# Kernel tuning notes

Measured on AMD Instinct MI355X. Metric: run time of the kernel, lower is better.

The kernel has to match this reference:

```python
import jax, jax.numpy as jnp
import numpy as np

IN_CH = 64
NODE = 48
K_NEIGS = 10
KERNEL = 5
STRIDE = 2
BN_EPS = 1e-5


def _local_kernel(size, k, s):
    idx = np.arange(size * size).reshape(size, size)
    win = np.lib.stride_tricks.sliding_window_view(idx, (k, k))[::s, ::s]
    patches = win.reshape(-1, k * k)  # [n_edges, k*k] pixel indices
    n_edges = patches.shape[0]
    H = np.zeros((size * size, n_edges), dtype=np.float32)
    H[patches.reshape(-1), np.repeat(np.arange(n_edges), k * k)] = 1.0
    return jnp.asarray(H)


def _pairwise_distance(x):
    # (B,N,C) -> (B,N,N) squared euclidean
    xsq = jnp.sum(x * x, axis=-1, keepdims=True)
    return xsq - 2.0 * jnp.einsum('bnc,bmc->bnm', x, x) + jnp.swapaxes(xsq, 1, 2)


def _batched_knn(x, k):
    d = _pairwise_distance(x)
    avg = d.mean(-1, keepdims=True)
    neg_vals, inds = jax.lax.top_k(-d, k + 1)  # smallest k+1, sorted ascending
    return -neg_vals, inds, d, avg


def _incidence(inds, N):
    # weights_function(prob=False) == ones; scatter ones then transpose
    B, _, K = inds.shape
    b = jnp.arange(B)[:, None, None]
    p = jnp.arange(N)[None, :, None]
    M = jnp.zeros((B, N, N), dtype=jnp.float32).at[b, p, inds].set(1.0)
    return jnp.swapaxes(M, 1, 2)


def _generate_G(H):
    # G = diag(DV^-0.5) @ H @ I @ diag(DE^-1) @ H^T @ diag(DV^-0.5)
    DV = H.sum(axis=2)  # (B,N)
    DE = H.sum(axis=1)  # (B,E)
    dv2 = DV ** -0.5
    Hs = H * (1.0 / DE)[:, None, :]
    M = jnp.einsum('bne,bme->bnm', Hs, H)
    return dv2[:, :, None] * M * dv2[:, None, :]


def _build_G(x, local_H):
    B, N, C = x.shape
    _, topk_inds, _, _ = _batched_knn(x, K_NEIGS)
    H1 = _incidence(topk_inds, N)
    Dv = H1.sum(axis=2, keepdims=True)  # alpha = 1.0
    max_k = int(jnp.max(Dv))  # data-dependent width (eager, matches torch)
    _, ti2, _, _ = _batched_knn(x, max_k - 1)  # (B,N,max_k)
    tk = jnp.arange(max_k)[None, None, :]
    rng = jnp.broadcast_to(jnp.arange(N)[None, :, None], (B, N, max_k))
    new_inds = jnp.where(tk >= Dv, rng, ti2)
    new_H = _incidence(new_inds, N)
    loc = jnp.broadcast_to(local_H[None], (B,) + local_H.shape)
    return _generate_G(jnp.concatenate([new_H, loc], axis=2))


def _hgnn(x, G, W, b, gamma, beta):
    h = jnp.einsum('bnc,oc->bno', x, W) + b  # Linear
    h = jnp.einsum('bnm,bmc->bnc', G, h)
    mean = h.mean(axis=(0, 1))  # BatchNorm1d over (B,N) per channel
    var = h.var(axis=(0, 1))
    h = gamma * (h - mean) / jnp.sqrt(var + BN_EPS) + beta
    return jax.nn.relu(h) + x


def setup_inputs() -> dict:
    key = jax.random.key(0)
    k1, k2, k3 = jax.random.split(key, 3)
    B, N, C = 4, NODE * NODE, IN_CH
    x = jax.random.normal(k1, (B, N, C), dtype=jnp.float32)
    W = jax.random.normal(k2, (C, C), dtype=jnp.float32) / np.sqrt(C)
    b = jax.random.normal(k3, (C,), dtype=jnp.float32) * 0.01
    gamma = jnp.ones((C,), dtype=jnp.float32)
    beta = jnp.zeros((C,), dtype=jnp.float32)
    return {"x": x, "W": W, "b": b, "gamma": gamma, "beta": beta}


def reference(x, W, b, gamma, beta):
    local_H = _local_kernel(NODE, KERNEL, STRIDE)
    G = _build_G(x, local_H)  # graph construction is no_grad in torch
    return _hgnn(x, G, W, b, gamma, beta)
```

## Files before the change

### kernel.cpp

```cpp
#include <hip/hip_runtime.h>


#define HB    4
#define HN    2304
#define HC    64
#define HK    11
#define HL    48
#define HW    22
#define HE2   484
#define HE    (HN + HE2)
#define HRPB  4
#define NSLOT 36
#define HCAP4 256
#define NPAIRS (HB * HK * HN)

__global__ void hg17_sentinel(float* out, int n) {
    int i = blockIdx.x * 256 + threadIdx.x;
    if (i < n) out[i] = 12345.0f;
}

__global__ void hg17_init(int* Dv, int* indeg, int* needfb, float* bnsum, float* bnss) {
    int i = blockIdx.x * 256 + threadIdx.x;
    if (i < HB * HN) { Dv[i] = 0; indeg[i] = 0; needfb[i] = 0; }
    if (i < HC) { bnsum[i] = 0.f; bnss[i] = 0.f; }
}

__global__ __launch_bounds__(256) void hg17_linear(const float* x, const float* W,
                                                   const float* bias, float* h1,
                                                   float* xsq, float* xT) {
    int wv = threadIdx.x >> 6, lane = threadIdx.x & 63;
    int row = blockIdx.x * 4 + wv;
    __shared__ float xr[4][HC];
    float v = x[row * HC + lane];
    xr[wv][lane] = v;
    __syncthreads();
    float sq = v * v;
    #pragma unroll
    for (int o = 32; o > 0; o >>= 1) sq += __shfl_xor(sq, o);
    if (lane == 0) xsq[row] = sq;
    int b = row / HN, n = row % HN;
    xT[(b * HC + lane) * HN + n] = v;
    float acc = bias[lane];
    #pragma unroll 8
    for (int c = 0; c < HC; c++) acc += xr[wv][c] * W[lane * HC + c];
    h1[row * HC + lane] = acc;
}

__device__ __forceinline__ unsigned hg17_wave_min_u32(unsigned v) {
    #pragma unroll
    for (int o = 32; o > 0; o >>= 1) {
        unsigned ov = __shfl_xor(v, o);
        v = ov < v ? ov : v;
    }
    return v;
}

#define HG17_INS4(q0, q1, q2, q3, x)                                     \
    {                                                                    \
        unsigned long long x_ = (x), n_;                                 \
        n_ = q0 < x_ ? q0 : x_; x_ = q0 < x_ ? x_ : q0; q0 = n_;         \
        n_ = q1 < x_ ? q1 : x_; x_ = q1 < x_ ? x_ : q1; q1 = n_;         \
        n_ = q2 < x_ ? q2 : x_; x_ = q2 < x_ ? x_ : q2; q2 = n_;         \
        if (x_ < q3) q3 = x_;                                            \
    }

#define HG17_CE(u, v)                                                    \
    { unsigned long long t_ = u < v ? u : v; v = u < v ? v : u; u = t_; }

#define HG17_BUILD()                                                               \
    {                                                                              \
        unsigned long long a0 = CINF, a1 = CINF, a2 = CINF, a3 = CINF;             \
        unsigned long long b0 = CINF, b1 = CINF, b2 = CINF, b3 = CINF;             \
        _Pragma("unroll")                                                          \
        for (int s = 0; s < NSLOT / 2; s++) {                                      \
            unsigned long long pa = ((unsigned long long)key[s] << 12) |           \
                                    (unsigned)((s << 6) | lane);                   \
            unsigned long long pb = ((unsigned long long)key[s + 18] << 12) |      \
                                    (unsigned)(((s + 18) << 6) | lane);            \
            HG17_INS4(a0, a1, a2, a3, pa);                                         \
            HG17_INS4(b0, b1, b2, b3, pb);                                         \
        }                                                                          \
        c0 = a0 < b3 ? a0 : b3; c1 = a1 < b2 ? a1 : b2;                            \
        c2 = a2 < b1 ? a2 : b1; c3 = a3 < b0 ? a3 : b0;                            \
        HG17_CE(c0, c2); HG17_CE(c1, c3); HG17_CE(c0, c1); HG17_CE(c2, c3);        \
    }

#define HG17_EXTRACT(kk, EMIT)                                                     \
    {                                                                              \
        for (int j = 0; j < (kk); j++) {                                           \
            unsigned hk = (unsigned)(c0 >> 12);                                    \
            unsigned mk = hg17_wave_min_u32(hk);                                   \
            unsigned long long bal = __ballot(hk == mk);                           \
            bool iswin;                                                            \
            if (__popcll(bal) == 1) {                                              \
                iswin = (hk == mk);                                                \
            } else {                                                               \
                unsigned mc = (hk == mk) ? (unsigned)(c0 & 0xFFFu) : 0xFFFFFFFFu;  \
                unsigned mm = hg17_wave_min_u32(mc);                               \
                iswin = (mc == mm);                                                \
            }                                                                      \
            if (iswin) {                                                           \
                int bi = (int)(c0 & 0xFFFu);                                       \
                EMIT;                                                              \
                unsigned long long popped = c0;                                    \
                c0 = c1; c1 = c2; c2 = c3; c3 = CINF;                              \
                if (c0 == CINF) {                                                  \
                    _Pragma("unroll")                                              \
                    for (int s = 0; s < NSLOT; s++) {                              \
                        unsigned long long pk =                                    \
                            ((unsigned long long)key[s] << 12) |                   \
                            (unsigned)((s << 6) | lane);                           \
                        if (pk > popped) HG17_INS4(c0, c1, c2, c3, pk);            \
                    }                                                              \
                }                                                                  \
            }                                                                      \
        }                                                                          \
    }

template <int NS>
__device__ __forceinline__ void hg17_kth(const unsigned (&key)[NS], int kk,
                                         unsigned& T, int& cntLess, int& take) {
    unsigned andv = 0xFFFFFFFFu, orv = 0u;
    #pragma unroll
    for (int s = 0; s < NS; s++) { andv &= key[s]; orv |= key[s]; }
    #pragma unroll
    for (int o = 32; o > 0; o >>= 1) {
        andv &= (unsigned)__shfl_xor((int)andv, o);
        orv  |= (unsigned)__shfl_xor((int)orv, o);
    }
    unsigned diff = andv ^ orv;
    if (diff == 0u) { T = andv; cntLess = 0; take = kk; return; }
    int tstart = 31 - __builtin_clz(diff);
    unsigned lowmask = (tstart == 31) ? 0xFFFFFFFFu : ((1u << (tstart + 1)) - 1u);
    unsigned pref = andv & ~lowmask;
    int r = kk;
    for (int t = tstart; t >= 0; t--) {
        unsigned pt = pref >> t;
        int c = 0;
        #pragma unroll
        for (int s = 0; s < NS; s++) c += ((key[s] >> t) == pt) ? 1 : 0;
        #pragma unroll
        for (int o = 32; o > 0; o >>= 1) c += __shfl_xor(c, o);
        if (r > c) { r -= c; pref |= (1u << t); }
    }
    T = pref; cntLess = kk - r; take = r;
}

__device__ __forceinline__ void hg17_scan64(int v, int lane, int& excl, int& total) {
    int inc = v;
    #pragma unroll
    for (int o = 1; o < 64; o <<= 1) {
        int u = __shfl_up(inc, o);
        if (lane >= o) inc += u;
    }
    excl = inc - v;
    total = __shfl(inc, 63);
}

__global__ __launch_bounds__(256) void hg17_knn_count(const float* xT, const float* xsq,
                                                      int* Dv, unsigned long long* topc) {
    __shared__ float d[HRPB][HN];
    __shared__ __align__(16) float xrt[HC][HRPB];
    const int t = threadIdx.x;
    const int b = blockIdx.x / (HN / HRPB);
    const int n0 = (blockIdx.x % (HN / HRPB)) * HRPB;
    const int r = t >> 6;
    const int lane = t & 63;
    xrt[lane][r] = xT[(b * HC + lane) * HN + n0 + r];
    __syncthreads();
    float xs[HRPB];
    #pragma unroll
    for (int q = 0; q < HRPB; q++) xs[q] = xsq[b * HN + n0 + q];

    #pragma unroll
    for (int i = 0; i < 4; i++) {
        const int m = 512 * i + 2 * t;
        float2 d0 = {0.f, 0.f}, d1 = {0.f, 0.f}, d2 = {0.f, 0.f}, d3 = {0.f, 0.f};
        #pragma unroll 8
        for (int c = 0; c < HC; c++) {
            float4 xq = *reinterpret_cast<const float4*>(&xrt[c][0]);
            float2 xv = *reinterpret_cast<const float2*>(&xT[(b * HC + c) * HN + m]);
            d0.x += xq.x * xv.x; d0.y += xq.x * xv.y;
            d1.x += xq.y * xv.x; d1.y += xq.y * xv.y;
            d2.x += xq.z * xv.x; d2.y += xq.z * xv.y;
            d3.x += xq.w * xv.x; d3.y += xq.w * xv.y;
        }
        float s0 = xsq[b * HN + m], s1 = xsq[b * HN + m + 1];
        *reinterpret_cast<float2*>(&d[0][m]) =
            make_float2(xs[0] + s0 - 2.f * d0.x, xs[0] + s1 - 2.f * d0.y);
        *reinterpret_cast<float2*>(&d[1][m]) =
            make_float2(xs[1] + s0 - 2.f * d1.x, xs[1] + s1 - 2.f * d1.y);
        *reinterpret_cast<float2*>(&d[2][m]) =
            make_float2(xs[2] + s0 - 2.f * d2.x, xs[2] + s1 - 2.f * d2.y);
        *reinterpret_cast<float2*>(&d[3][m]) =
            make_float2(xs[3] + s0 - 2.f * d3.x, xs[3] + s1 - 2.f * d3.y);
    }
    {
        const int m = 2048 + t;
        float d0 = 0.f, d1 = 0.f, d2 = 0.f, d3 = 0.f;
        #pragma unroll 8
        for (int c = 0; c < HC; c++) {
            float4 xq = *reinterpret_cast<const float4*>(&xrt[c][0]);
            float xv = xT[(b * HC + c) * HN + m];
            d0 += xq.x * xv; d1 += xq.y * xv; d2 += xq.z * xv; d3 += xq.w * xv;
        }
        float sm = xsq[b * HN + m];
        d[0][m] = xs[0] + sm - 2.f * d0;
        d[1][m] = xs[1] + sm - 2.f * d1;
        d[2][m] = xs[2] + sm - 2.f * d2;
        d[3][m] = xs[3] + sm - 2.f * d3;
    }
    __syncthreads();

    const int p = n0 + r;
    const int gw = b * HN + p;
    const unsigned long long CINF = ~0ull;
    unsigned int key[NSLOT];
    unsigned long long c0, c1, c2, c3;
    #pragma unroll
    for (int s = 0; s < NSLOT; s++) {
        float f = d[r][(s << 6) | lane];
        unsigned int ub = __float_as_uint(f);
        key[s] = ub ^ (((unsigned int)(((int)ub) >> 31)) | 0x80000000u);
    }
    HG17_BUILD();
    {
        unsigned long long* tb = topc + (size_t)gw * HCAP4;
        tb[lane]       = c0;
        tb[64 + lane]  = c1;
        tb[128 + lane] = c2;
        tb[192 + lane] = c3;
    }
    HG17_EXTRACT(HK, atomicAdd(&Dv[b * HN + bi], 1));
}

__global__ __launch_bounds__(256) void hg17_scan(const int* Dv, int* offs) {
    __shared__ int part[256];
    int t = threadIdx.x;
    int base = t * 36;
    int s = 0;
    for (int i = 0; i < 36; i++) s += max(Dv[base + i], 1);
    part[t] = s;
    __syncthreads();
    if (t == 0) { int acc = 0; for (int i = 0; i < 256; i++) { int v = part[i]; part[i] = acc; acc += v; } }
    __syncthreads();
    int acc = part[t];
    for (int i = 0; i < 36; i++) { offs[base + i] = acc; acc += max(Dv[base + i], 1); }
}

__global__ __launch_bounds__(256) void hg17_sel_top(const unsigned long long* topc,
                                                    const int* Dv, const int* offs,
                                                    int* needfb, int* indeg,
                                                    unsigned int* pairs) {
    const int t = threadIdx.x;
    const int lane = t & 63;
    const int gw = blockIdx.x * HRPB + (t >> 6);
    const int b = gw / HN, p = gw % HN;
    const int kk = max(Dv[gw], 1);
    unsigned long long pk[4];
    unsigned key[4];
    #pragma unroll
    for (int s = 0; s < 4; s++) {
        pk[s] = topc[(size_t)gw * HCAP4 + (s << 6) + lane];
        key[s] = (unsigned)(pk[s] >> 12);
    }
    if (kk > HCAP4) {
        if (lane == 0) needfb[gw] = 1;
        return;
    }
    unsigned T; int cntLess, take;
    hg17_kth<4>(key, kk, T, cntLess, take);
    unsigned long long bad = __ballot(key[3] <= T);
    if (bad != 0ull) {
        if (lane == 0) needfb[gw] = 1;
        return;
    }
    const int base = offs[gw];
    int cl = 0;
    #pragma unroll
    for (int s = 0; s < 4; s++) cl += (key[s] < T) ? 1 : 0;
    int off, tot;
    hg17_scan64(cl, lane, off, tot);
    int w = 0;
    #pragma unroll
    for (int s = 0; s < 4; s++) {
        if (key[s] < T) {
            int m = (int)(pk[s] & 0xFFFu);
            atomicAdd(&indeg[b * HN + m], 1);
            pairs[base + off + w] =
                ((unsigned)b << 24) | ((unsigned)p << 12) | (unsigned)m;
            w++;
        }
    }
    int lastm = -1;
    for (int t2 = 0; t2 < take; t2++) {
        int mc = 0x7FFFFFFF;
        #pragma unroll
        for (int s = 0; s < 4; s++) {
            int m = (int)(pk[s] & 0xFFFu);
            if (key[s] == T && m > lastm && m < mc) mc = m;
        }
        int mmin = mc;
        #pragma unroll
        for (int o = 32; o > 0; o >>= 1) {
            int ov = __shfl_xor(mmin, o);
            mmin = ov < mmin ? ov : mmin;
        }
        if (mc == mmin) {
            atomicAdd(&indeg[b * HN + mmin], 1);
            pairs[base + cntLess + t2] =
                ((unsigned)b << 24) | ((unsigned)p << 12) | (unsigned)mmin;
        }
        lastm = mmin;
    }
}

__global__ __launch_bounds__(256) void hg17_sel_fullfb(const float* xT, const float* xsq,
                                                       const int* Dv, const int* offs,
                                                       const int* needfb, int* indeg,
                                                       unsigned int* pairs) {
    const int t = threadIdx.x;
    const int b = blockIdx.x / (HN / HRPB);
    const int n0 = (blockIdx.x % (HN / HRPB)) * HRPB;
    bool need = false;
    #pragma unroll
    for (int q = 0; q < HRPB; q++) need |= (needfb[b * HN + n0 + q] != 0);
    if (!need) return;

    __shared__ float d[HRPB][HN];
    __shared__ float xr[HRPB][HC];
    const int r = t >> 6;
    const int lane = t & 63;
    xr[r][lane] = xT[(b * HC + lane) * HN + n0 + r];
    __syncthreads();
    float xs[HRPB];
    #pragma unroll
    for (int q = 0; q < HRPB; q++) xs[q] = xsq[b * HN + n0 + q];
    for (int m = t; m < HN; m += 256) {
        float dot0 = 0.f, dot1 = 0.f, dot2 = 0.f, dot3 = 0.f;
        #pragma unroll 8
        for (int c = 0; c < HC; c++) {
            float xv = xT[(b * HC + c) * HN + m];
            dot0 += xr[0][c] * xv;
            dot1 += xr[1][c] * xv;
            dot2 += xr[2][c] * xv;
            dot3 += xr[3][c] * xv;
        }
        float xsm = xsq[b * HN + m];
        d[0][m] = xs[0] + xsm - 2.f * dot0;
        d[1][m] = xs[1] + xsm - 2.f * dot1;
        d[2][m] = xs[2] + xsm - 2.f * dot2;
        d[3][m] = xs[3] + xsm - 2.f * dot3;
    }
    __syncthreads();
    const int p = n0 + r;
    const int gw = b * HN + p;
    if (needfb[gw] == 0) return;
    const int kk = max(Dv[gw], 1);
    unsigned int key[NSLOT];
    #pragma unroll
    for (int s = 0; s < NSLOT; s++) {
        float f = d[r][(s << 6) | lane];
        unsigned int ub = __float_as_uint(f);
        key[s] = ub ^ (((unsigned int)(((int)ub) >> 31)) | 0x80000000u);
    }
    unsigned T; int cntLess, take;
    hg17_kth<NSLOT>(key, kk, T, cntLess, take);
    const int base = offs[gw];
    int cl = 0;
    #pragma unroll
    for (int s = 0; s < NSLOT; s++) cl += (key[s] < T) ? 1 : 0;
    int off, tot;
    hg17_scan64(cl, lane, off, tot);
    int w = 0;
    #pragma unroll
    for (int s = 0; s < NSLOT; s++) {
        if (key[s] < T) {
            int m = (s << 6) | lane;
            atomicAdd(&indeg[b * HN + m], 1);
            pairs[base + off + w] =
                ((unsigned)b << 24) | ((unsigned)p << 12) | (unsigned)m;
            w++;
        }
    }
    int lastm = -1;
    for (int t2 = 0; t2 < take; t2++) {
        int mc = 0x7FFFFFFF;
        #pragma unroll
        for (int s = 0; s < NSLOT; s++) {
            int m = (s << 6) | lane;
            if (key[s] == T && m > lastm && m < mc) mc = m;
        }
        int mmin = mc;
        #pragma unroll
        for (int o = 32; o > 0; o >>= 1) {
            int ov = __shfl_xor(mmin, o);
            mmin = ov < mmin ? ov : mmin;
        }
        if (mc == mmin) {
            atomicAdd(&indeg[b * HN + mmin], 1);
            pairs[base + cntLess + t2] =
                ((unsigned)b << 24) | ((unsigned)p << 12) | (unsigned)mmin;
        }
        lastm = mmin;
    }
}

__device__ __forceinline__ int hg17_lo(int rc) { return max(0, (rc - 3) / 2); }
__device__ __forceinline__ int hg17_hi(int rc) { return min(HW - 1, rc / 2); }

__global__ __launch_bounds__(256) void hg17_prep(float* h1, const int* indeg,
                                                 float* z, float* h2) {
    int i = blockIdx.x * 256 + threadIdx.x;
    int node = i >> 6;
    int n = node % HN;
    int r = n / HL, c = n % HL;
    int cover = max(0, hg17_hi(r) - hg17_lo(r) + 1) * max(0, hg17_hi(c) - hg17_lo(c) + 1);
    int dvn = max(indeg[node] + cover, 1);
    h1[i] *= rsqrtf((float)dvn);
    int b = i / (HN * HC), rem = i % (HN * HC);
    z[b * HE * HC + rem] = 0.f;
    h2[i] = 0.f;
}

__global__ __launch_bounds__(256) void hg17_edge(const unsigned int* pairs, const int* Dv,
                                                 const float* y, float* z) {
    int wv = (blockIdx.x * 256 + threadIdx.x) >> 6;
    int lane = threadIdx.x & 63;
    if (wv < NPAIRS) {
        unsigned int pk = pairs[wv];
        int b = pk >> 24;
        if (b >= HB) return;
        int p = (pk >> 12) & 0xFFF, m = pk & 0xFFF;
        float invde = 1.f / (float)max(Dv[b * HN + p], 1);
        atomicAdd(&z[(b * HE + p) * HC + lane], y[(b * HN + m) * HC + lane] * invde);
    } else {
        int w2 = wv - NPAIRS;
        if (w2 >= HB * HE2) return;
        int b = w2 / HE2, w = w2 % HE2;
        int wr = w / HW, wc = w % HW;
        float acc = 0.f;
        #pragma unroll
        for (int i = 0; i < 5; i++)
            #pragma unroll
            for (int j = 0; j < 5; j++)
                acc += y[(b * HN + (wr * 2 + i) * HL + wc * 2 + j) * HC + lane];
        z[(b * HE + HN + w) * HC + lane] = acc * (1.f / 25.f);
    }
}

__global__ __launch_bounds__(256) void hg17_gscatter(const unsigned int* pairs,
                                                     const float* z, float* h2) {
    int idx = (blockIdx.x * 256 + threadIdx.x) >> 6;
    int lane = threadIdx.x & 63;
    if (idx >= NPAIRS) return;
    unsigned int pk = pairs[idx];
    int b = pk >> 24;
    if (b >= HB) return;
    int p = (pk >> 12) & 0xFFF, m = pk & 0xFFF;
    atomicAdd(&h2[(b * HN + m) * HC + lane], z[(b * HE + p) * HC + lane]);
}

__global__ __launch_bounds__(256) void hg17_gfinish(const float* z, const int* indeg, float* h2) {
    int wave = (blockIdx.x * 256 + threadIdx.x) >> 6;
    int lane = threadIdx.x & 63;
    int b = wave / HN, n = wave % HN;
    int g = b * HN + n;
    float acc = h2[g * HC + lane];
    int r = n / HL, c = n % HL;
    int rlo = hg17_lo(r), rhi = hg17_hi(r), clo = hg17_lo(c), chi = hg17_hi(c);
    for (int wr = rlo; wr <= rhi; wr++)
        for (int wc = clo; wc <= chi; wc++)
            acc += z[(b * HE + HN + wr * HW + wc) * HC + lane];
    int dvn = max(indeg[g] + max(0, rhi - rlo + 1) * max(0, chi - clo + 1), 1);
    h2[g * HC + lane] = acc * rsqrtf((float)dvn);
}

__global__ __launch_bounds__(256) void hg17_bnstats(const float* h2, float* bnsum, float* bnss) {
    int t = threadIdx.x;
    int c = t & 63, rg = t >> 6;
    int row0 = blockIdx.x * 36;
    float s = 0.f, ss = 0.f;
    for (int r = rg; r < 36; r += 4) {
        float v = h2[(row0 + r) * HC + c];
        s += v; ss += v * v;
    }
    __shared__ float ls[256], lss[256];
    ls[t] = s; lss[t] = ss;
    __syncthreads();
    if (t < 64) {
        s  = ls[t]  + ls[t + 64]  + ls[t + 128]  + ls[t + 192];
        ss = lss[t] + lss[t + 64] + lss[t + 128] + lss[t + 192];
        atomicAdd(&bnsum[t], s);
        atomicAdd(&bnss[t], ss);
    }
}

__global__ __launch_bounds__(256) void hg17_final(const float* h2, const float* x,
                                                  const float* gamma, const float* beta,
                                                  const float* bnsum, const float* bnss,
                                                  float* out) {
    int i = blockIdx.x * 256 + threadIdx.x;
    int c = i & 63;
    const float M = (float)(HB * HN);
    float mean = bnsum[c] / M;
    float var  = bnss[c] / M - mean * mean;
    float inv  = rsqrtf(var + 1e-5f);
    float h = gamma[c] * (h2[i] - mean) * inv + beta[c];
    out[i] = fmaxf(h, 0.f) + x[i];
}

extern "C" void kernel_launch(void* const* d_in, const int* in_sizes, int n_in,
                              void* d_out, int out_size, void* d_ws, size_t ws_size,
                              hipStream_t stream) {
    const float* x     = (const float*)d_in[0];
    const float* W     = (const float*)d_in[1];
    const float* bias  = (const float*)d_in[2];
    const float* gamma = (const float*)d_in[3];
    const float* beta  = (const float*)d_in[4];
    float* out = (float*)d_out;
    (void)in_sizes; (void)n_in;

    char* ws = (char*)d_ws;
    size_t off = 0;
    float*              xsq    = (float*)(ws + off);              off += (size_t)HB * HN * 4;
    float*              h1     = (float*)(ws + off);              off += (size_t)HB * HN * HC * 4;
    float*              h2     = (float*)(ws + off);              off += (size_t)HB * HN * HC * 4;
    int*                Dv     = (int*)(ws + off);                off += (size_t)HB * HN * 4;
    int*                indeg  = (int*)(ws + off);                off += (size_t)HB * HN * 4;
    int*                offs   = (int*)(ws + off);                off += (size_t)HB * HN * 4;
    int*                needfb = (int*)(ws + off);                off += (size_t)HB * HN * 4;
    unsigned int*       pairs  = (unsigned int*)(ws + off);       off += (size_t)NPAIRS * 4;
    float*              bnsum  = (float*)(ws + off);              off += 256;
    float*              bnss   = (float*)(ws + off);              off += 256;
    unsigned long long* topc   = (unsigned long long*)(ws + off); off += (size_t)HB * HN * HCAP4 * 8;
    float*              xT     = (float*)(ws + off);
    float*              z      = (float*)(ws + off);
    off += (size_t)HB * HE * HC * 4;

    if (ws_size < off) {
        hg17_sentinel<<<(out_size + 255) / 256, 256, 0, stream>>>(out, out_size);
        return;
    }

    const int EDGE_WAVES = NPAIRS + HB * HE2;

    hg17_init<<<(HB * HN + 255) / 256, 256, 0, stream>>>(Dv, indeg, needfb, bnsum, bnss);
    hg17_linear<<<HB * HN / 4, 256, 0, stream>>>(x, W, bias, h1, xsq, xT);
    hg17_knn_count<<<HB * (HN / HRPB), 256, 0, stream>>>(xT, xsq, Dv, topc);
    hg17_scan<<<1, 256, 0, stream>>>(Dv, offs);
    hg17_sel_top<<<HB * (HN / HRPB), 256, 0, stream>>>(topc, Dv, offs, needfb, indeg, pairs);
    hg17_sel_fullfb<<<HB * (HN / HRPB), 256, 0, stream>>>(xT, xsq, Dv, offs, needfb, indeg, pairs);
    hg17_prep<<<(HB * HN * HC) / 256, 256, 0, stream>>>(h1, indeg, z, h2);
    hg17_edge<<<EDGE_WAVES / 4, 256, 0, stream>>>(pairs, Dv, h1, z);
    hg17_gscatter<<<(NPAIRS * 64) / 256, 256, 0, stream>>>(pairs, z, h2);
    hg17_gfinish<<<(HB * HN) / 4, 256, 0, stream>>>(z, indeg, h2);
    hg17_bnstats<<<256, 256, 0, stream>>>(h2, bnsum, bnss);
    hg17_final<<<(HB * HN * HC) / 256, 256, 0, stream>>>(h2, x, gamma, beta, bnsum, bnss, out);
}
```

Before: 385.5 us.

## Replace atomic scatter with CSR gather for hypergraph propagation; widen top-k cache to 8

```diff
diff --git a/kernel.cpp b/kernel.cpp
--- a/kernel.cpp
+++ b/kernel.cpp
@@ -11,21 +11,22 @@
 #define HE    (HN + HE2)
 #define HRPB  4
 #define NSLOT 36
-#define HCAP4 256
+#define HCAP8 512
 #define NPAIRS (HB * HK * HN)
 
-__global__ void hg17_sentinel(float* out, int n) {
+__global__ void hg18_sentinel(float* out, int n) {
     int i = blockIdx.x * 256 + threadIdx.x;
     if (i < n) out[i] = 12345.0f;
 }
 
-__global__ void hg17_init(int* Dv, int* indeg, int* needfb, float* bnsum, float* bnss) {
+__global__ void hg18_init(int* Dv, int* indeg, int* cursor, int* needfb,
+                          float* bnsum, float* bnss) {
     int i = blockIdx.x * 256 + threadIdx.x;
-    if (i < HB * HN) { Dv[i] = 0; indeg[i] = 0; needfb[i] = 0; }
+    if (i < HB * HN) { Dv[i] = 0; indeg[i] = 0; cursor[i] = 0; needfb[i] = 0; }
     if (i < HC) { bnsum[i] = 0.f; bnss[i] = 0.f; }
 }
 
-__global__ __launch_bounds__(256) void hg17_linear(const float* x, const float* W,
+__global__ __launch_bounds__(256) void hg18_linear(const float* x, const float* W,
                                                    const float* bias, float* h1,
                                                    float* xsq, float* xT) {
     int wv = threadIdx.x >> 6, lane = threadIdx.x & 63;
@@ -46,7 +47,7 @@
     h1[row * HC + lane] = acc;
 }
 
-__device__ __forceinline__ unsigned hg17_wave_min_u32(unsigned v) {
+__device__ __forceinline__ unsigned hg18_wave_min_u32(unsigned v) {
     #pragma unroll
     for (int o = 32; o > 0; o >>= 1) {
         unsigned ov = __shfl_xor(v, o);
@@ -55,7 +56,7 @@
     return v;
 }
 
-#define HG17_INS4(q0, q1, q2, q3, x)                                     \
+#define HG18_INS4(q0, q1, q2, q3, x)                                     \
     {                                                                    \
         unsigned long long x_ = (x), n_;                                 \
         n_ = q0 < x_ ? q0 : x_; x_ = q0 < x_ ? x_ : q0; q0 = n_;         \
@@ -64,39 +65,21 @@
         if (x_ < q3) q3 = x_;                                            \
     }
 
-#define HG17_CE(u, v)                                                    \
+#define HG18_CE(u, v)                                                    \
     { unsigned long long t_ = u < v ? u : v; v = u < v ? v : u; u = t_; }
 
-#define HG17_BUILD()                                                               \
-    {                                                                              \
-        unsigned long long a0 = CINF, a1 = CINF, a2 = CINF, a3 = CINF;             \
-        unsigned long long b0 = CINF, b1 = CINF, b2 = CINF, b3 = CINF;             \
-        _Pragma("unroll")                                                          \
-        for (int s = 0; s < NSLOT / 2; s++) {                                      \
-            unsigned long long pa = ((unsigned long long)key[s] << 12) |           \
-                                    (unsigned)((s << 6) | lane);                   \
-            unsigned long long pb = ((unsigned long long)key[s + 18] << 12) |      \
-                                    (unsigned)(((s + 18) << 6) | lane);            \
-            HG17_INS4(a0, a1, a2, a3, pa);                                         \
-            HG17_INS4(b0, b1, b2, b3, pb);                                         \
-        }                                                                          \
-        c0 = a0 < b3 ? a0 : b3; c1 = a1 < b2 ? a1 : b2;                            \
-        c2 = a2 < b1 ? a2 : b1; c3 = a3 < b0 ? a3 : b0;                            \
-        HG17_CE(c0, c2); HG17_CE(c1, c3); HG17_CE(c0, c1); HG17_CE(c2, c3);        \
-    }
-
-#define HG17_EXTRACT(kk, EMIT)                                                     \
+#define HG18_EXTRACT(kk, EMIT)                                                     \
     {                                                                              \
         for (int j = 0; j < (kk); j++) {                                           \
             unsigned hk = (unsigned)(c0 >> 12);                                    \
-            unsigned mk = hg17_wave_min_u32(hk);                                   \
+            unsigned mk = hg18_wave_min_u32(hk);                                   \
             unsigned long long bal = __ballot(hk == mk);                           \
             bool iswin;                                                            \
             if (__popcll(bal) == 1) {                                              \
                 iswin = (hk == mk);                                                \
             } else {                                                               \
                 unsigned mc = (hk == mk) ? (unsigned)(c0 & 0xFFFu) : 0xFFFFFFFFu;  \
-                unsigned mm = hg17_wave_min_u32(mc);                               \
+                unsigned mm = hg18_wave_min_u32(mc);                               \
                 iswin = (mc == mm);                                                \
             }                                                                      \
             if (iswin) {                                                           \
@@ -110,7 +93,7 @@
                         unsigned long long pk =                                    \
                             ((unsigned long long)key[s] << 12) |                   \
                             (unsigned)((s << 6) | lane);                           \
-                        if (pk > popped) HG17_INS4(c0, c1, c2, c3, pk);            \
+                        if (pk > popped) HG18_INS4(c0, c1, c2, c3, pk);            \
                     }                                                              \
                 }                                                                  \
             }                                                                      \
@@ -118,7 +101,7 @@
     }
 
 template <int NS>
-__device__ __forceinline__ void hg17_kth(const unsigned (&key)[NS], int kk,
+__device__ __forceinline__ void hg18_kth(const unsigned (&key)[NS], int kk,
                                          unsigned& T, int& cntLess, int& take) {
     unsigned andv = 0xFFFFFFFFu, orv = 0u;
     #pragma unroll
@@ -146,7 +129,7 @@
     T = pref; cntLess = kk - r; take = r;
 }
 
-__device__ __forceinline__ void hg17_scan64(int v, int lane, int& excl, int& total) {
+__device__ __forceinline__ void hg18_scan64(int v, int lane, int& excl, int& total) {
     int inc = v;
     #pragma unroll
     for (int o = 1; o < 64; o <<= 1) {
@@ -157,7 +140,7 @@
     total = __shfl(inc, 63);
 }
 
-__global__ __launch_bounds__(256) void hg17_knn_count(const float* xT, const float* xsq,
+__global__ __launch_bounds__(256) void hg18_knn_count(const float* xT, const float* xsq,
                                                       int* Dv, unsigned long long* topc) {
     __shared__ float d[HRPB][HN];
     __shared__ __align__(16) float xrt[HC][HRPB];
@@ -223,32 +206,66 @@
         unsigned int ub = __float_as_uint(f);
         key[s] = ub ^ (((unsigned int)(((int)ub) >> 31)) | 0x80000000u);
     }
-    HG17_BUILD();
     {
-        unsigned long long* tb = topc + (size_t)gw * HCAP4;
-        tb[lane]       = c0;
-        tb[64 + lane]  = c1;
-        tb[128 + lane] = c2;
-        tb[192 + lane] = c3;
-    }
-    HG17_EXTRACT(HK, atomicAdd(&Dv[b * HN + bi], 1));
-}
-
-__global__ __launch_bounds__(256) void hg17_scan(const int* Dv, int* offs) {
+        unsigned long long a0 = CINF, a1 = CINF, a2 = CINF, a3 = CINF;
+        unsigned long long b0 = CINF, b1 = CINF, b2 = CINF, b3 = CINF;
+        #pragma unroll
+        for (int s = 0; s < NSLOT / 2; s++) {
+            unsigned long long pa = ((unsigned long long)key[s] << 12) |
+                                    (unsigned)((s << 6) | lane);
+            unsigned long long pb = ((unsigned long long)key[s + 18] << 12) |
+                                    (unsigned)(((s + 18) << 6) | lane);
+            HG18_INS4(a0, a1, a2, a3, pa);
+            HG18_INS4(b0, b1, b2, b3, pb);
+        }
+        c0 = a0 < b3 ? a0 : b3; c1 = a1 < b2 ? a1 : b2;
+        c2 = a2 < b1 ? a2 : b1; c3 = a3 < b0 ? a3 : b0;
+        HG18_CE(c0, c2); HG18_CE(c1, c3); HG18_CE(c0, c1); HG18_CE(c2, c3);
+    }
+    unsigned long long* tb = topc + (size_t)gw * HCAP8;
+    tb[lane]       = c0;
+    tb[64 + lane]  = c1;
+    tb[128 + lane] = c2;
+    tb[192 + lane] = c3;
+    {
+        unsigned long long lo = c3;
+        unsigned long long a0 = CINF, a1 = CINF, a2 = CINF, a3 = CINF;
+        unsigned long long b0 = CINF, b1 = CINF, b2 = CINF, b3 = CINF;
+        #pragma unroll
+        for (int s = 0; s < NSLOT / 2; s++) {
+            unsigned long long pa = ((unsigned long long)key[s] << 12) |
+                                    (unsigned)((s << 6) | lane);
+            unsigned long long pb = ((unsigned long long)key[s + 18] << 12) |
+                                    (unsigned)(((s + 18) << 6) | lane);
+            if (pa > lo) HG18_INS4(a0, a1, a2, a3, pa);
+            if (pb > lo) HG18_INS4(b0, b1, b2, b3, pb);
+        }
+        unsigned long long q4 = a0 < b3 ? a0 : b3, q5 = a1 < b2 ? a1 : b2;
+        unsigned long long q6 = a2 < b1 ? a2 : b1, q7 = a3 < b0 ? a3 : b0;
+        HG18_CE(q4, q6); HG18_CE(q5, q7); HG18_CE(q4, q5); HG18_CE(q6, q7);
+        tb[256 + lane] = q4;
+        tb[320 + lane] = q5;
+        tb[384 + lane] = q6;
+        tb[448 + lane] = q7;
+    }
+    HG18_EXTRACT(HK, atomicAdd(&Dv[b * HN + bi], 1));
+}
+
+__global__ __launch_bounds__(256) void hg18_scan(const int* v, int* out, int clamp1) {
     __shared__ int part[256];
     int t = threadIdx.x;
     int base = t * 36;
     int s = 0;
-    for (int i = 0; i < 36; i++) s += max(Dv[base + i], 1);
+    for (int i = 0; i < 36; i++) s += clamp1 ? max(v[base + i], 1) : v[base + i];
     part[t] = s;
     __syncthreads();
-    if (t == 0) { int acc = 0; for (int i = 0; i < 256; i++) { int v = part[i]; part[i] = acc; acc += v; } }
+    if (t == 0) { int acc = 0; for (int i = 0; i < 256; i++) { int q = part[i]; part[i] = acc; acc += q; } }
     __syncthreads();
     int acc = part[t];
-    for (int i = 0; i < 36; i++) { offs[base + i] = acc; acc += max(Dv[base + i], 1); }
-}
-
-__global__ __launch_bounds__(256) void hg17_sel_top(const unsigned long long* topc,
+    for (int i = 0; i < 36; i++) { out[base + i] = acc; acc += clamp1 ? max(v[base + i], 1) : v[base + i]; }
+}
+
+__global__ __launch_bounds__(256) void hg18_sel_top(const unsigned long long* topc,
                                                     const int* Dv, const int* offs,
                                                     int* needfb, int* indeg,
                                                     unsigned int* pairs) {
@@ -257,20 +274,20 @@
     const int gw = blockIdx.x * HRPB + (t >> 6);
     const int b = gw / HN, p = gw % HN;
     const int kk = max(Dv[gw], 1);
-    unsigned long long pk[4];
-    unsigned key[4];
-    #pragma unroll
-    for (int s = 0; s < 4; s++) {
-        pk[s] = topc[(size_t)gw * HCAP4 + (s << 6) + lane];
+    unsigned long long pk[8];
+    unsigned key[8];
+    #pragma unroll
+    for (int s = 0; s < 8; s++) {
+        pk[s] = topc[(size_t)gw * HCAP8 + (s << 6) + lane];
         key[s] = (unsigned)(pk[s] >> 12);
     }
-    if (kk > HCAP4) {
+    if (kk > HCAP8) {
         if (lane == 0) needfb[gw] = 1;
         return;
     }
     unsigned T; int cntLess, take;
-    hg17_kth<4>(key, kk, T, cntLess, take);
-    unsigned long long bad = __ballot(key[3] <= T);
+    hg18_kth<8>(key, kk, T, cntLess, take);
+    unsigned long long bad = __ballot(key[7] <= T);
     if (bad != 0ull) {
         if (lane == 0) needfb[gw] = 1;
         return;
@@ -278,12 +295,12 @@
     const int base = offs[gw];
     int cl = 0;
     #pragma unroll
-    for (int s = 0; s < 4; s++) cl += (key[s] < T) ? 1 : 0;
+    for (int s = 0; s < 8; s++) cl += (key[s] < T) ? 1 : 0;
     int off, tot;
-    hg17_scan64(cl, lane, off, tot);
+    hg18_scan64(cl, lane, off, tot);
     int w = 0;
     #pragma unroll
-    for (int s = 0; s < 4; s++) {
+    for (int s = 0; s < 8; s++) {
         if (key[s] < T) {
             int m = (int)(pk[s] & 0xFFFu);
             atomicAdd(&indeg[b * HN + m], 1);
@@ -296,7 +313,7 @@
     for (int t2 = 0; t2 < take; t2++) {
         int mc = 0x7FFFFFFF;
         #pragma unroll
-        for (int s = 0; s < 4; s++) {
+        for (int s = 0; s < 8; s++) {
             int m = (int)(pk[s] & 0xFFFu);
             if (key[s] == T && m > lastm && m < mc) mc = m;
         }
@@ -315,7 +332,7 @@
     }
 }
 
-__global__ __launch_bounds__(256) void hg17_sel_fullfb(const float* xT, const float* xsq,
+__global__ __launch_bounds__(256) void hg18_sel_fullfb(const float* xT, const float* xsq,
                                                        const int* Dv, const int* offs,
                                                        const int* needfb, int* indeg,
                                                        unsigned int* pairs) {
@@ -365,13 +382,13 @@
         key[s] = ub ^ (((unsigned int)(((int)ub) >> 31)) | 0x80000000u);
     }
     unsigned T; int cntLess, take;
-    hg17_kth<NSLOT>(key, kk, T, cntLess, take);
+    hg18_kth<NSLOT>(key, kk, T, cntLess, take);
     const int base = offs[gw];
     int cl = 0;
     #pragma unroll
     for (int s = 0; s < NSLOT; s++) cl += (key[s] < T) ? 1 : 0;
     int off, tot;
-    hg17_scan64(cl, lane, off, tot);
+    hg18_scan64(cl, lane, off, tot);
     int w = 0;
     #pragma unroll
     for (int s = 0; s < NSLOT; s++) {
@@ -406,77 +423,91 @@
     }
 }
 
-__device__ __forceinline__ int hg17_lo(int rc) { return max(0, (rc - 3) / 2); }
-__device__ __forceinline__ int hg17_hi(int rc) { return min(HW - 1, rc / 2); }
-
-__global__ __launch_bounds__(256) void hg17_prep(float* h1, const int* indeg,
-                                                 float* z, float* h2) {
+__global__ __launch_bounds__(256) void hg18_transpose(const unsigned int* pairs,
+                                                      const int* moffs, int* cursor,
+                                                      unsigned short* inlist) {
+    int idx = blockIdx.x * 256 + threadIdx.x;
+    if (idx >= NPAIRS) return;
+    unsigned pk = pairs[idx];
+    int b = pk >> 24;
+    if (b >= HB) return;
+    int p = (pk >> 12) & 0xFFF, m = pk & 0xFFF;
+    int g = b * HN + m;
+    int slot = atomicAdd(&cursor[g], 1);
+    inlist[moffs[g] + slot] = (unsigned short)p;
+}
+
+__device__ __forceinline__ int hg18_lo(int rc) { return max(0, (rc - 3) / 2); }
+__device__ __forceinline__ int hg18_hi(int rc) { return min(HW - 1, rc / 2); }
+
+__global__ __launch_bounds__(256) void hg18_prep(float* h1, const int* indeg) {
     int i = blockIdx.x * 256 + threadIdx.x;
     int node = i >> 6;
     int n = node % HN;
     int r = n / HL, c = n % HL;
-    int cover = max(0, hg17_hi(r) - hg17_lo(r) + 1) * max(0, hg17_hi(c) - hg17_lo(c) + 1);
+    int cover = max(0, hg18_hi(r) - hg18_lo(r) + 1) * max(0, hg18_hi(c) - hg18_lo(c) + 1);
     int dvn = max(indeg[node] + cover, 1);
     h1[i] *= rsqrtf((float)dvn);
-    int b = i / (HN * HC), rem = i % (HN * HC);
-    z[b * HE * HC + rem] = 0.f;
-    h2[i] = 0.f;
-}
-
-__global__ __launch_bounds__(256) void hg17_edge(const unsigned int* pairs, const int* Dv,
-                                                 const float* y, float* z) {
+}
+
+__global__ __launch_bounds__(256) void hg18_edge(const unsigned int* pairs, const int* Dv,
+                                                 const int* offs, const float* y, float* z) {
     int wv = (blockIdx.x * 256 + threadIdx.x) >> 6;
     int lane = threadIdx.x & 63;
-    if (wv < NPAIRS) {
-        unsigned int pk = pairs[wv];
-        int b = pk >> 24;
-        if (b >= HB) return;
-        int p = (pk >> 12) & 0xFFF, m = pk & 0xFFF;
-        float invde = 1.f / (float)max(Dv[b * HN + p], 1);
-        atomicAdd(&z[(b * HE + p) * HC + lane], y[(b * HN + m) * HC + lane] * invde);
+    int b = wv / HE, e = wv % HE;
+    float acc = 0.f;
+    if (e < HN) {
+        int gw = b * HN + e;
+        int kk = max(Dv[gw], 1);
+        int base = offs[gw];
+        for (int j0 = 0; j0 < kk; j0 += 64) {
+            unsigned pk = (j0 + lane < kk) ? pairs[base + j0 + lane] : 0u;
+            int lim = min(64, kk - j0);
+            for (int j = 0; j < lim; j++) {
+                int m = (int)(__shfl(pk, j) & 0xFFFu);
+                acc += y[(b * HN + m) * HC + lane];
+            }
+        }
+        acc *= 1.f / (float)kk;
     } else {
-        int w2 = wv - NPAIRS;
-        if (w2 >= HB * HE2) return;
-        int b = w2 / HE2, w = w2 % HE2;
-        int wr = w / HW, wc = w % HW;
-        float acc = 0.f;
+        int w = e - HN; int wr = w / HW, wc = w % HW;
         #pragma unroll
         for (int i = 0; i < 5; i++)
             #pragma unroll
             for (int j = 0; j < 5; j++)
                 acc += y[(b * HN + (wr * 2 + i) * HL + wc * 2 + j) * HC + lane];
-        z[(b * HE + HN + w) * HC + lane] = acc * (1.f / 25.f);
-    }
-}
-
-__global__ __launch_bounds__(256) void hg17_gscatter(const unsigned int* pairs,
-                                                     const float* z, float* h2) {
-    int idx = (blockIdx.x * 256 + threadIdx.x) >> 6;
+        acc *= (1.f / 25.f);
+    }
+    z[(b * HE + e) * HC + lane] = acc;
+}
+
+__global__ __launch_bounds__(256) void hg18_node(const float* z, const int* indeg,
+                                                 const int* moffs, const unsigned short* inlist,
+                                                 float* h2) {
+    int wv = (blockIdx.x * 256 + threadIdx.x) >> 6;
     int lane = threadIdx.x & 63;
-    if (idx >= NPAIRS) return;
-    unsigned int pk = pairs[idx];
-    int b = pk >> 24;
-    if (b >= HB) return;
-    int p = (pk >> 12) & 0xFFF, m = pk & 0xFFF;
-    atomicAdd(&h2[(b * HN + m) * HC + lane], z[(b * HE + p) * HC + lane]);
-}
-
-__global__ __launch_bounds__(256) void hg17_gfinish(const float* z, const int* indeg, float* h2) {
-    int wave = (blockIdx.x * 256 + threadIdx.x) >> 6;
-    int lane = threadIdx.x & 63;
-    int b = wave / HN, n = wave % HN;
+    int b = wv / HN, n = wv % HN;
     int g = b * HN + n;
-    float acc = h2[g * HC + lane];
+    int cnt = indeg[g], off = moffs[g];
+    float acc = 0.f;
+    for (int j0 = 0; j0 < cnt; j0 += 64) {
+        int pv = (j0 + lane < cnt) ? (int)inlist[off + j0 + lane] : 0;
+        int lim = min(64, cnt - j0);
+        for (int j = 0; j < lim; j++) {
+            int p = __shfl(pv, j);
+            acc += z[(b * HE + p) * HC + lane];
+        }
+    }
     int r = n / HL, c = n % HL;
-    int rlo = hg17_lo(r), rhi = hg17_hi(r), clo = hg17_lo(c), chi = hg17_hi(c);
+    int rlo = hg18_lo(r), rhi = hg18_hi(r), clo = hg18_lo(c), chi = hg18_hi(c);
     for (int wr = rlo; wr <= rhi; wr++)
         for (int wc = clo; wc <= chi; wc++)
             acc += z[(b * HE + HN + wr * HW + wc) * HC + lane];
-    int dvn = max(indeg[g] + max(0, rhi - rlo + 1) * max(0, chi - clo + 1), 1);
+    int dvn = max(cnt + max(0, rhi - rlo + 1) * max(0, chi - clo + 1), 1);
     h2[g * HC + lane] = acc * rsqrtf((float)dvn);
 }
 
-__global__ __launch_bounds__(256) void hg17_bnstats(const float* h2, float* bnsum, float* bnss) {
+__global__ __launch_bounds__(256) void hg18_bnstats(const float* h2, float* bnsum, float* bnss) {
     int t = threadIdx.x;
     int c = t & 63, rg = t >> 6;
     int row0 = blockIdx.x * 36;
@@ -496,7 +527,7 @@
     }
 }
 
-__global__ __launch_bounds__(256) void hg17_final(const float* h2, const float* x,
+__global__ __launch_bounds__(256) void hg18_final(const float* h2, const float* x,
                                                   const float* gamma, const float* beta,
                                                   const float* bnsum, const float* bnss,
                                                   float* out) {
@@ -529,32 +560,34 @@
     int*                Dv     = (int*)(ws + off);                off += (size_t)HB * HN * 4;
     int*                indeg  = (int*)(ws + off);                off += (size_t)HB * HN * 4;
     int*                offs   = (int*)(ws + off);                off += (size_t)HB * HN * 4;
+    int*                moffs  = (int*)(ws + off);                off += (size_t)HB * HN * 4;
+    int*                cursor = (int*)(ws + off);                off += (size_t)HB * HN * 4;
     int*                needfb = (int*)(ws + off);                off += (size_t)HB * HN * 4;
     unsigned int*       pairs  = (unsigned int*)(ws + off);       off += (size_t)NPAIRS * 4;
+    unsigned short*     inlist = (unsigned short*)(ws + off);     off += (size_t)NPAIRS * 2;
     float*              bnsum  = (float*)(ws + off);              off += 256;
     float*              bnss   = (float*)(ws + off);              off += 256;
-    unsigned long long* topc   = (unsigned long long*)(ws + off); off += (size_t)HB * HN * HCAP4 * 8;
+    unsigned long long* topc   = (unsigned long long*)(ws + off); off += (size_t)HB * HN * HCAP8 * 8;
     float*              xT     = (float*)(ws + off);
     float*              z      = (float*)(ws + off);
     off += (size_t)HB * HE * HC * 4;
 
     if (ws_size < off) {
-        hg17_sentinel<<<(out_size + 255) / 256, 256, 0, stream>>>(out, out_size);
+        hg18_sentinel<<<(out_size + 255) / 256, 256, 0, stream>>>(out, out_size);
         return;
     }
 
-    const int EDGE_WAVES = NPAIRS + HB * HE2;
-
-    hg17_init<<<(HB * HN + 255) / 256, 256, 0, stream>>>(Dv, indeg, needfb, bnsum, bnss);
-    hg17_linear<<<HB * HN / 4, 256, 0, stream>>>(x, W, bias, h1, xsq, xT);
-    hg17_knn_count<<<HB * (HN / HRPB), 256, 0, stream>>>(xT, xsq, Dv, topc);
-    hg17_scan<<<1, 256, 0, stream>>>(Dv, offs);
-    hg17_sel_top<<<HB * (HN / HRPB), 256, 0, stream>>>(topc, Dv, offs, needfb, indeg, pairs);
-    hg17_sel_fullfb<<<HB * (HN / HRPB), 256, 0, stream>>>(xT, xsq, Dv, offs, needfb, indeg, pairs);
-    hg17_prep<<<(HB * HN * HC) / 256, 256, 0, stream>>>(h1, indeg, z, h2);
-    hg17_edge<<<EDGE_WAVES / 4, 256, 0, stream>>>(pairs, Dv, h1, z);
-    hg17_gscatter<<<(NPAIRS * 64) / 256, 256, 0, stream>>>(pairs, z, h2);
-    hg17_gfinish<<<(HB * HN) / 4, 256, 0, stream>>>(z, indeg, h2);
-    hg17_bnstats<<<256, 256, 0, stream>>>(h2, bnsum, bnss);
-    hg17_final<<<(HB * HN * HC) / 256, 256, 0, stream>>>(h2, x, gamma, beta, bnsum, bnss, out);
-}
+    hg18_init<<<(HB * HN + 255) / 256, 256, 0, stream>>>(Dv, indeg, cursor, needfb, bnsum, bnss);
+    hg18_linear<<<HB * HN / 4, 256, 0, stream>>>(x, W, bias, h1, xsq, xT);
+    hg18_knn_count<<<HB * (HN / HRPB), 256, 0, stream>>>(xT, xsq, Dv, topc);
+    hg18_scan<<<1, 256, 0, stream>>>(Dv, offs, 1);
+    hg18_sel_top<<<HB * (HN / HRPB), 256, 0, stream>>>(topc, Dv, offs, needfb, indeg, pairs);
+    hg18_sel_fullfb<<<HB * (HN / HRPB), 256, 0, stream>>>(xT, xsq, Dv, offs, needfb, indeg, pairs);
+    hg18_scan<<<1, 256, 0, stream>>>(indeg, moffs, 0);
+    hg18_transpose<<<(NPAIRS + 255) / 256, 256, 0, stream>>>(pairs, moffs, cursor, inlist);
+    hg18_prep<<<(HB * HN * HC) / 256, 256, 0, stream>>>(h1, indeg);
+    hg18_edge<<<(HB * HE) / 4, 256, 0, stream>>>(pairs, Dv, offs, h1, z);
+    hg18_node<<<(HB * HN) / 4, 256, 0, stream>>>(z, indeg, moffs, inlist, h2);
+    hg18_bnstats<<<256, 256, 0, stream>>>(h2, bnsum, bnss);
+    hg18_final<<<(HB * HN * HC) / 256, 256, 0, stream>>>(h2, x, gamma, beta, bnsum, bnss, out);
+}
```

After: 423.1 us. 1.1x slower.
